# Performance work log

Measured on AMD Instinct MI355X. Metric: run time of the kernel, lower is better.

Reference implementation:

```python
import jax, jax.numpy as jnp
import numpy as np

B, T, D, U = 32, 2048, 512, 512

def setup_inputs() -> dict:
    key = jax.random.key(0)
    ks = jax.random.split(key, 8)
    s = 0.02
    return {
        "query": jax.random.normal(ks[0], (B, D), dtype=jnp.float32),
        "values": jax.random.normal(ks[1], (B, T, D), dtype=jnp.float32),
        "W1_w": jax.random.normal(ks[2], (D, U), dtype=jnp.float32) * s,
        "W1_b": jnp.zeros((U,), dtype=jnp.float32),
        "W2_w": jax.random.normal(ks[3], (D, U), dtype=jnp.float32) * s,
        "W2_b": jnp.zeros((U,), dtype=jnp.float32),
        "V_w": jax.random.normal(ks[4], (U, 1), dtype=jnp.float32) * s,
        "V_b": jnp.zeros((1,), dtype=jnp.float32),
    }

def reference(query, values, W1_w, W1_b, W2_w, W2_b, V_w, V_b):
    # query: [B, D] -> [B, 1, U]; values: [B, T, D] -> [B, T, U]
    q_proj = (query @ W1_w + W1_b)[:, None, :]              # [B, 1, U]
    v_proj = jnp.einsum('btd,du->btu', values, W2_w) + W2_b  # [B, T, U]
    score = jnp.tanh(q_proj + v_proj) @ V_w + V_b            # [B, T, 1]
    attn = jax.nn.softmax(score, axis=1)                     # [B, T, 1]
    context = jnp.sum(attn * values, axis=1)                 # [B, D]
    return context, attn
```

## Files before the change

### kernel.cpp

```cpp
#include <hip/hip_runtime.h>
#include <hip/hip_bf16.h>
#include <cstddef>
#include <cstdint>

#define B_ 32
#define T_ 2048
#define D_ 512
#define U_ 512

typedef __attribute__((ext_vector_type(8))) short bf16x8;
typedef __attribute__((ext_vector_type(4))) float f32x4;

__device__ __forceinline__ unsigned short f2bf(float f) {
  union { float f; unsigned u; } x; x.f = f;
  unsigned r = x.u + 0x7fffu + ((x.u >> 16) & 1u);
  return (unsigned short)(r >> 16);
}
__device__ __forceinline__ float tanh_fast(float x) {
  float e = __expf(2.0f * x);
  return 1.0f - 2.0f * __builtin_amdgcn_rcpf(e + 1.0f);
}

#define AS1C(p) ((const __attribute__((address_space(1))) unsigned*)(p))
#define AS3(p)  ((__attribute__((address_space(3))) unsigned*)(p))

__device__ __forceinline__ void wave0_sumabs_vw(const float* __restrict__ Vw,
                                                float* Cs, int tid) {
  if (tid < 64) {
    float c = 0.f;
    #pragma unroll
    for (int i = 0; i < 8; ++i) c += fabsf(Vw[tid + i * 64]);
    c += __shfl_xor(c, 1);  c += __shfl_xor(c, 2);  c += __shfl_xor(c, 4);
    c += __shfl_xor(c, 8);  c += __shfl_xor(c, 16); c += __shfl_xor(c, 32);
    if (tid == 0) *Cs = c;
  }
}

__global__ void kA_prep(const float* __restrict__ W2, unsigned* __restrict__ W2P,
                        const float* __restrict__ query, const float* __restrict__ W1,
                        const float* __restrict__ W1b, const float* __restrict__ W2b,
                        float* __restrict__ qp, float* __restrict__ ctx) {
  const int tid = threadIdx.x;
  if (blockIdx.x < 64) {
    const int kg = blockIdx.x >> 2, q4 = blockIdx.x & 3;
    __shared__ unsigned short w2s[8][514];
    const float4* W2v = (const float4*)(W2 + (size_t)(kg * 32 + q4 * 8) * U_);
    #pragma unroll
    for (int i = 0; i < 4; ++i) {
      int idx4 = i * 256 + tid;
      float4 v = W2v[idx4];
      int r = idx4 >> 7, c = (idx4 & 127) * 4;
      w2s[r][c + 0] = f2bf(v.x); w2s[r][c + 1] = f2bf(v.y);
      w2s[r][c + 2] = f2bf(v.z); w2s[r][c + 3] = f2bf(v.w);
    }
    __syncthreads();
    const int idx = tid & 63;
    const int lr = (idx >> 2) & 15, j = idx & 3;
    const int kb = j * 2;
    #pragma unroll
    for (int r = 0; r < 8; ++r) {
      int ut = r * 4 + (tid >> 6);
      W2P[ut * 4096 + kg * 256 + q4 * 64 + idx] =
          (unsigned)w2s[kb][ut * 16 + lr] | ((unsigned)w2s[kb + 1][ut * 16 + lr] << 16);
    }
  } else {
    __shared__ float qs[D_];
    __shared__ float red[4][64];
    const int blk2 = blockIdx.x - 64;
    const int b = blk2 >> 3, us = blk2 & 7;
    const int ul = tid & 63, dq = tid >> 6;
    const int u = us * 64 + ul;
    qs[tid] = query[b * D_ + tid];
    qs[tid + 256] = query[b * D_ + tid + 256];
    __syncthreads();
    float a0 = 0, a1 = 0, a2 = 0, a3 = 0;
    const int d0 = dq * 128;
    for (int d = 0; d < 128; d += 4) {
      a0 += qs[d0 + d + 0] * W1[(size_t)(d0 + d + 0) * U_ + u];
      a1 += qs[d0 + d + 1] * W1[(size_t)(d0 + d + 1) * U_ + u];
      a2 += qs[d0 + d + 2] * W1[(size_t)(d0 + d + 2) * U_ + u];
      a3 += qs[d0 + d + 3] * W1[(size_t)(d0 + d + 3) * U_ + u];
    }
    red[dq][ul] = (a0 + a1) + (a2 + a3);
    __syncthreads();
    if (dq == 0) {
      float s = red[0][ul] + red[1][ul] + red[2][ul] + red[3][ul];
      qp[b * U_ + u] = s + W1b[u] + W2b[u];
    }
    if (tid < 64) ctx[blk2 * 64 + tid] = 0.0f;
  }
}

__global__ __launch_bounds__(512, 4) void k2attn(
    const float* __restrict__ values, const unsigned short* __restrict__ W2P,
    const float* __restrict__ qp, const float* __restrict__ Vw,
    float* __restrict__ score, float* __restrict__ ctxU) {
  __shared__ __align__(16) float av[2][4096];
  __shared__ float sred[8][64];
  __shared__ float ps2[64];
  __shared__ float Cs;

  const int tid = threadIdx.x;
  const int bx = blockIdx.x;
  const int m0 = bx * 64;
  const int b = m0 >> 11;
  const int l = tid & 63, w = tid >> 6;
  const int lr = l & 15, lq = l >> 4;

  const int r0 = tid >> 4;
  const int c0 = tid & 15;
  const float* vsrc0 = values + (size_t)(m0 + r0) * D_ + (c0 ^ (r0 & 15)) * 4;
  const float* vsrc1 = values + (size_t)(m0 + 32 + r0) * D_ + (c0 ^ (r0 & 15)) * 4;

  f32x4 acc[4][4];
  #pragma unroll
  for (int mi = 0; mi < 4; ++mi)
    #pragma unroll
    for (int ni = 0; ni < 4; ++ni) acc[mi][ni] = (f32x4){0.f, 0.f, 0.f, 0.f};

  const unsigned short* Bb = W2P + (size_t)(w * 4) * 8192 + (size_t)l * 8;

  auto stage = [&](int e, int p) {
    __builtin_amdgcn_global_load_lds(AS1C(vsrc0 + e * 64), AS3(&av[p][(r0) * 64 + ((tid & 15) << 2)]), 16, 0, 0);
    __builtin_amdgcn_global_load_lds(AS1C(vsrc1 + e * 64), AS3(&av[p][(32 + r0) * 64 + ((tid & 15) << 2)]), 16, 0, 0);
  };

  wave0_sumabs_vw(Vw, &Cs, tid);

  bf16x8 Bc[4], Bn[4];
  stage(0, 0);
  #pragma unroll
  for (int ni = 0; ni < 4; ++ni) Bc[ni] = *(const bf16x8*)(Bb + (size_t)ni * 8192);

  for (int kg = 0; kg < 16; ++kg) {
    const int e = kg >> 1, p = e & 1;
    if ((kg & 1) == 0) {
      __syncthreads();
      if (e < 7) stage(e + 1, p ^ 1);
    }
    if (kg < 15) {
      #pragma unroll
      for (int ni = 0; ni < 4; ++ni)
        Bn[ni] = *(const bf16x8*)(Bb + (size_t)ni * 8192 + (size_t)(kg + 1) * 512);
    }
    const int kq = kg & 1;
    const int p0 = (kq * 8 + lq * 2) ^ lr;
    bf16x8 a[4];
    #pragma unroll
    for (int mi = 0; mi < 4; ++mi) {
      const int row = mi * 16 + lr;
      f32x4 flo = *(const f32x4*)&av[p][row * 64 + (p0 << 2)];
      f32x4 fhi = *(const f32x4*)&av[p][row * 64 + ((p0 ^ 1) << 2)];
      union { bf16x8 v; __hip_bfloat162 h[4]; } A;
      A.h[0] = __float22bfloat162_rn(make_float2(flo.x, flo.y));
      A.h[1] = __float22bfloat162_rn(make_float2(flo.z, flo.w));
      A.h[2] = __float22bfloat162_rn(make_float2(fhi.x, fhi.y));
      A.h[3] = __float22bfloat162_rn(make_float2(fhi.z, fhi.w));
      a[mi] = A.v;
    }
    #pragma unroll
    for (int ni = 0; ni < 4; ++ni)
      #pragma unroll
      for (int mi = 0; mi < 4; ++mi)
        acc[mi][ni] = __builtin_amdgcn_mfma_f32_16x16x32_bf16(a[mi], Bc[ni], acc[mi][ni], 0, 0, 0);
    #pragma unroll
    for (int ni = 0; ni < 4; ++ni) Bc[ni] = Bn[ni];
  }

  float sacc[4][4];
  #pragma unroll
  for (int mi = 0; mi < 4; ++mi)
    #pragma unroll
    for (int r = 0; r < 4; ++r) sacc[mi][r] = 0.0f;
  #pragma unroll
  for (int ni = 0; ni < 4; ++ni) {
    int u = (w * 4 + ni) * 16 + lr;
    float qpv = qp[b * U_ + u], vv = Vw[u];
    #pragma unroll
    for (int mi = 0; mi < 4; ++mi)
      #pragma unroll
      for (int r = 0; r < 4; ++r)
        sacc[mi][r] += tanh_fast(acc[mi][ni][r] + qpv) * vv;
  }
  #pragma unroll
  for (int mi = 0; mi < 4; ++mi)
    #pragma unroll
    for (int r = 0; r < 4; ++r) {
      float v = sacc[mi][r];
      v += __shfl_xor(v, 1); v += __shfl_xor(v, 2);
      v += __shfl_xor(v, 4); v += __shfl_xor(v, 8);
      if (lr == 0) sred[w][mi * 16 + lq * 4 + r] = v;
    }
  __syncthreads();

  if (tid < 64) {
    float s = 0.f;
    #pragma unroll
    for (int wv = 0; wv < 8; ++wv) s += sred[wv][tid];
    score[m0 + tid] = s;
    ps2[tid] = __expf(s - Cs);
  }
  __syncthreads();

  float accc = 0.f;
  const int col = tid;
  #pragma unroll 4
  for (int row = 0; row < 64; ++row)
    accc += ps2[row] * values[(size_t)(m0 + row) * D_ + col];
  atomicAdd(&ctxU[(size_t)b * D_ + col], accc);
}

__global__ void kB_final(const float* __restrict__ Vw, float* __restrict__ attn,
                         float* __restrict__ ctx) {
  __shared__ float Cs;
  __shared__ float red[4];
  const int b = blockIdx.x, tid = threadIdx.x;
  wave0_sumabs_vw(Vw, &Cs, tid);
  __syncthreads();
  const float C = Cs;
  float* s = attn + b * T_;
  float p[8];
  float sum = 0.f;
  #pragma unroll
  for (int i = 0; i < 8; ++i) { p[i] = __expf(s[tid + i * 256] - C); sum += p[i]; }
  #pragma unroll
  for (int off = 1; off < 64; off <<= 1) sum += __shfl_xor(sum, off);
  if ((tid & 63) == 0) red[tid >> 6] = sum;
  __syncthreads();
  sum = (red[0] + red[1]) + (red[2] + red[3]);
  const float inv = 1.0f / sum;
  #pragma unroll
  for (int i = 0; i < 8; ++i) attn[b * T_ + tid + i * 256] = p[i] * inv;
  #pragma unroll
  for (int i = 0; i < 2; ++i) ctx[b * D_ + tid + i * 256] *= inv;
}

extern "C" void kernel_launch(void* const* d_in, const int* in_sizes, int n_in,
                              void* d_out, int out_size, void* d_ws, size_t ws_size,
                              hipStream_t stream) {
  const float* query = (const float*)d_in[0];
  const float* values = (const float*)d_in[1];
  const float* W1w = (const float*)d_in[2];
  const float* W1b = (const float*)d_in[3];
  const float* W2w = (const float*)d_in[4];
  const float* W2b = (const float*)d_in[5];
  const float* Vw  = (const float*)d_in[6];

  float* out = (float*)d_out;
  float* ctx  = out;
  float* attn = out + B_ * D_;
  float* score = attn;

  char* ws = (char*)d_ws;
  unsigned* W2P = (unsigned*)ws;
  float* qp    = (float*)(ws + 512 * 1024);

  kA_prep<<<320, 256, 0, stream>>>(W2w, W2P, query, W1w, W1b, W2b, qp, ctx);
  k2attn<<<1024, 512, 0, stream>>>(values, (const unsigned short*)W2P, qp, Vw, score, ctx);
  kB_final<<<32, 256, 0, stream>>>(Vw, attn, ctx);
}
```

Before: 242.0 us.

## Load A operand directly from global memory instead of LDS staging

Removes the double-buffered LDS staging of the values tile via global_load_lds and its per-stage barriers. Each wave now reads its fp32 A fragments straight from global memory, converts them to bf16, and fully unrolls the k loop with per-iteration B loads. This drops LDS traffic and synchronisation, but every one of the 8 waves now re-reads the same 64-row values tile from global/L2, so redundant global loads go up. The explicit B register prefetch is also removed.

```diff
diff --git a/kernel.cpp b/kernel.cpp
--- a/kernel.cpp
+++ b/kernel.cpp
@@ -20,9 +20,6 @@
   float e = __expf(2.0f * x);
   return 1.0f - 2.0f * __builtin_amdgcn_rcpf(e + 1.0f);
 }
-
-#define AS1C(p) ((const __attribute__((address_space(1))) unsigned*)(p))
-#define AS3(p)  ((__attribute__((address_space(3))) unsigned*)(p))
 
 __device__ __forceinline__ void wave0_sumabs_vw(const float* __restrict__ Vw,
                                                 float* Cs, int tid) {
@@ -91,11 +88,20 @@
   }
 }
 
+#define LOADA(dst, base)                                                  \
+  { f32x4 flo = *(const f32x4*)((base) + kg * 32);                        \
+    f32x4 fhi = *(const f32x4*)((base) + kg * 32 + 4);                    \
+    union { bf16x8 v; __hip_bfloat162 h[4]; } Au;                         \
+    Au.h[0] = __float22bfloat162_rn(make_float2(flo.x, flo.y));           \
+    Au.h[1] = __float22bfloat162_rn(make_float2(flo.z, flo.w));           \
+    Au.h[2] = __float22bfloat162_rn(make_float2(fhi.x, fhi.y));           \
+    Au.h[3] = __float22bfloat162_rn(make_float2(fhi.z, fhi.w));           \
+    dst = Au.v; }
+
 __global__ __launch_bounds__(512, 4) void k2attn(
     const float* __restrict__ values, const unsigned short* __restrict__ W2P,
     const float* __restrict__ qp, const float* __restrict__ Vw,
     float* __restrict__ score, float* __restrict__ ctxU) {
-  __shared__ __align__(16) float av[2][4096];
   __shared__ float sred[8][64];
   __shared__ float ps2[64];
   __shared__ float Cs;
@@ -107,11 +113,6 @@
   const int l = tid & 63, w = tid >> 6;
   const int lr = l & 15, lq = l >> 4;
 
-  const int r0 = tid >> 4;
-  const int c0 = tid & 15;
-  const float* vsrc0 = values + (size_t)(m0 + r0) * D_ + (c0 ^ (r0 & 15)) * 4;
-  const float* vsrc1 = values + (size_t)(m0 + 32 + r0) * D_ + (c0 ^ (r0 & 15)) * 4;
-
   f32x4 acc[4][4];
   #pragma unroll
   for (int mi = 0; mi < 4; ++mi)
@@ -119,52 +120,28 @@
     for (int ni = 0; ni < 4; ++ni) acc[mi][ni] = (f32x4){0.f, 0.f, 0.f, 0.f};
 
   const unsigned short* Bb = W2P + (size_t)(w * 4) * 8192 + (size_t)l * 8;
-
-  auto stage = [&](int e, int p) {
-    __builtin_amdgcn_global_load_lds(AS1C(vsrc0 + e * 64), AS3(&av[p][(r0) * 64 + ((tid & 15) << 2)]), 16, 0, 0);
-    __builtin_amdgcn_global_load_lds(AS1C(vsrc1 + e * 64), AS3(&av[p][(32 + r0) * 64 + ((tid & 15) << 2)]), 16, 0, 0);
-  };
+  const float* a0p = values + (size_t)(m0 + lr) * D_ + lq * 8;
+  const float* a1p = a0p + (size_t)16 * D_;
+  const float* a2p = a0p + (size_t)32 * D_;
+  const float* a3p = a0p + (size_t)48 * D_;
 
   wave0_sumabs_vw(Vw, &Cs, tid);
 
-  bf16x8 Bc[4], Bn[4];
-  stage(0, 0);
-  #pragma unroll
-  for (int ni = 0; ni < 4; ++ni) Bc[ni] = *(const bf16x8*)(Bb + (size_t)ni * 8192);
-
+  #pragma unroll
   for (int kg = 0; kg < 16; ++kg) {
-    const int e = kg >> 1, p = e & 1;
-    if ((kg & 1) == 0) {
-      __syncthreads();
-      if (e < 7) stage(e + 1, p ^ 1);
-    }
-    if (kg < 15) {
-      #pragma unroll
-      for (int ni = 0; ni < 4; ++ni)
-        Bn[ni] = *(const bf16x8*)(Bb + (size_t)ni * 8192 + (size_t)(kg + 1) * 512);
-    }
-    const int kq = kg & 1;
-    const int p0 = (kq * 8 + lq * 2) ^ lr;
-    bf16x8 a[4];
-    #pragma unroll
-    for (int mi = 0; mi < 4; ++mi) {
-      const int row = mi * 16 + lr;
-      f32x4 flo = *(const f32x4*)&av[p][row * 64 + (p0 << 2)];
-      f32x4 fhi = *(const f32x4*)&av[p][row * 64 + ((p0 ^ 1) << 2)];
-      union { bf16x8 v; __hip_bfloat162 h[4]; } A;
-      A.h[0] = __float22bfloat162_rn(make_float2(flo.x, flo.y));
-      A.h[1] = __float22bfloat162_rn(make_float2(flo.z, flo.w));
-      A.h[2] = __float22bfloat162_rn(make_float2(fhi.x, fhi.y));
-      A.h[3] = __float22bfloat162_rn(make_float2(fhi.z, fhi.w));
-      a[mi] = A.v;
-    }
+    bf16x8 Bv[4];
     #pragma unroll
     for (int ni = 0; ni < 4; ++ni)
-      #pragma unroll
-      for (int mi = 0; mi < 4; ++mi)
-        acc[mi][ni] = __builtin_amdgcn_mfma_f32_16x16x32_bf16(a[mi], Bc[ni], acc[mi][ni], 0, 0, 0);
-    #pragma unroll
-    for (int ni = 0; ni < 4; ++ni) Bc[ni] = Bn[ni];
+      Bv[ni] = *(const bf16x8*)(Bb + (size_t)ni * 8192 + (size_t)kg * 512);
+    bf16x8 af0, af1, af2, af3;
+    LOADA(af0, a0p); LOADA(af1, a1p); LOADA(af2, a2p); LOADA(af3, a3p);
+    #pragma unroll
+    for (int ni = 0; ni < 4; ++ni) {
+      acc[0][ni] = __builtin_amdgcn_mfma_f32_16x16x32_bf16(af0, Bv[ni], acc[0][ni], 0, 0, 0);
+      acc[1][ni] = __builtin_amdgcn_mfma_f32_16x16x32_bf16(af1, Bv[ni], acc[1][ni], 0, 0, 0);
+      acc[2][ni] = __builtin_amdgcn_mfma_f32_16x16x32_bf16(af2, Bv[ni], acc[2][ni], 0, 0, 0);
+      acc[3][ni] = __builtin_amdgcn_mfma_f32_16x16x32_bf16(af3, Bv[ni], acc[3][ni], 0, 0, 0);
+    }
   }
 
   float sacc[4][4];
```

New measurement: 357.8 us. 47.9% more time.

## Stage values tile as bf16 in LDS via register prefetch instead of direct fp32 loads

Applied to the files above, without the earlier changes.

Replaces the direct global-to-LDS fp32 staging of the values tile with register-prefetched global loads that are converted to bf16 once and written into a swizzled 64x128 bf16 LDS buffer. Each k-stage now covers 128 columns, processed as four stages of four MFMA k-groups with two register prefetch buffers. This removes the per-wave repeated fp32-to-bf16 conversion and halves LDS footprint and read traffic. In exchange it uses more VGPRs for the prefetch registers, which is why the occupancy hint drops from 4 to 3 blocks per CU, and it gives up the asynchronous load-to-LDS path.

```diff
diff --git a/kernel.cpp b/kernel.cpp
--- a/kernel.cpp
+++ b/kernel.cpp
@@ -20,9 +20,11 @@
   float e = __expf(2.0f * x);
   return 1.0f - 2.0f * __builtin_amdgcn_rcpf(e + 1.0f);
 }
-
-#define AS1C(p) ((const __attribute__((address_space(1))) unsigned*)(p))
-#define AS3(p)  ((__attribute__((address_space(3))) unsigned*)(p))
+__device__ __forceinline__ unsigned packbf2(float a, float b) {
+  union { __hip_bfloat162 h; unsigned u; } c;
+  c.h = __float22bfloat162_rn(make_float2(a, b));
+  return c.u;
+}
 
 __device__ __forceinline__ void wave0_sumabs_vw(const float* __restrict__ Vw,
                                                 float* Cs, int tid) {
@@ -91,11 +93,11 @@
   }
 }
 
-__global__ __launch_bounds__(512, 4) void k2attn(
+__global__ __launch_bounds__(512, 3) void k2attn(
     const float* __restrict__ values, const unsigned short* __restrict__ W2P,
     const float* __restrict__ qp, const float* __restrict__ Vw,
     float* __restrict__ score, float* __restrict__ ctxU) {
-  __shared__ __align__(16) float av[2][4096];
+  __shared__ __align__(16) unsigned short av[2][64][128];
   __shared__ float sred[8][64];
   __shared__ float ps2[64];
   __shared__ float Cs;
@@ -107,10 +109,12 @@
   const int l = tid & 63, w = tid >> 6;
   const int lr = l & 15, lq = l >> 4;
 
-  const int r0 = tid >> 4;
-  const int c0 = tid & 15;
-  const float* vsrc0 = values + (size_t)(m0 + r0) * D_ + (c0 ^ (r0 & 15)) * 4;
-  const float* vsrc1 = values + (size_t)(m0 + 32 + r0) * D_ + (c0 ^ (r0 & 15)) * 4;
+  const int r_st = tid >> 3;
+  const int s0 = (tid & 7) * 2;
+  const int r15 = r_st & 15;
+  const float* gsrc = values + (size_t)(m0 + r_st) * D_ + s0 * 8;
+  char* wd0 = (char*)&av[0][r_st][0] + ((s0 ^ r15) << 4);
+  char* wd1 = (char*)&av[0][r_st][0] + (((s0 + 1) ^ r15) << 4);
 
   f32x4 acc[4][4];
   #pragma unroll
@@ -120,51 +124,64 @@
 
   const unsigned short* Bb = W2P + (size_t)(w * 4) * 8192 + (size_t)l * 8;
 
-  auto stage = [&](int e, int p) {
-    __builtin_amdgcn_global_load_lds(AS1C(vsrc0 + e * 64), AS3(&av[p][(r0) * 64 + ((tid & 15) << 2)]), 16, 0, 0);
-    __builtin_amdgcn_global_load_lds(AS1C(vsrc1 + e * 64), AS3(&av[p][(32 + r0) * 64 + ((tid & 15) << 2)]), 16, 0, 0);
+  float4 La[4], Lb[4];
+  auto loadG = [&](float4* L, int q) {
+    const float4* g = (const float4*)(gsrc + q * 128);
+    L[0] = g[0]; L[1] = g[1]; L[2] = g[2]; L[3] = g[3];
   };
+  auto writeL = [&](int p, const float4* L) {
+    uint4 w0 = make_uint4(packbf2(L[0].x, L[0].y), packbf2(L[0].z, L[0].w),
+                          packbf2(L[1].x, L[1].y), packbf2(L[1].z, L[1].w));
+    uint4 w1 = make_uint4(packbf2(L[2].x, L[2].y), packbf2(L[2].z, L[2].w),
+                          packbf2(L[3].x, L[3].y), packbf2(L[3].z, L[3].w));
+    *(uint4*)(wd0 + p * 16384) = w0;
+    *(uint4*)(wd1 + p * 16384) = w1;
+  };
 
   wave0_sumabs_vw(Vw, &Cs, tid);
 
+  loadG(La, 0);
+  writeL(0, La);
+  loadG(Lb, 1);
+  __syncthreads();
+
   bf16x8 Bc[4], Bn[4];
-  stage(0, 0);
   #pragma unroll
   for (int ni = 0; ni < 4; ++ni) Bc[ni] = *(const bf16x8*)(Bb + (size_t)ni * 8192);
 
-  for (int kg = 0; kg < 16; ++kg) {
-    const int e = kg >> 1, p = e & 1;
-    if ((kg & 1) == 0) {
+  #pragma unroll
+  for (int q = 0; q < 4; ++q) {
+    const int p = q & 1;
+    if (q == 0) loadG(La, 2);
+    else if (q == 1) loadG(Lb, 3);
+    const char* buf = (const char*)av[p];
+    #pragma unroll
+    for (int kgl = 0; kgl < 4; ++kgl) {
+      const int kg = q * 4 + kgl;
+      if (kg < 15) {
+        #pragma unroll
+        for (int ni = 0; ni < 4; ++ni)
+          Bn[ni] = *(const bf16x8*)(Bb + (size_t)ni * 8192 + (size_t)(kg + 1) * 512);
+      }
+      bf16x8 a[4];
+      #pragma unroll
+      for (int mi = 0; mi < 4; ++mi) {
+        const int row = mi * 16 + lr;
+        const int phys = (kgl * 4 + lq) ^ lr;
+        a[mi] = *(const bf16x8*)(buf + row * 256 + (phys << 4));
+      }
+      #pragma unroll
+      for (int ni = 0; ni < 4; ++ni)
+        #pragma unroll
+        for (int mi = 0; mi < 4; ++mi)
+          acc[mi][ni] = __builtin_amdgcn_mfma_f32_16x16x32_bf16(a[mi], Bc[ni], acc[mi][ni], 0, 0, 0);
+      #pragma unroll
+      for (int ni = 0; ni < 4; ++ni) Bc[ni] = Bn[ni];
+    }
+    if (q < 3) {
+      writeL(p ^ 1, (q & 1) ? La : Lb);
       __syncthreads();
-      if (e < 7) stage(e + 1, p ^ 1);
-    }
-    if (kg < 15) {
-      #pragma unroll
-      for (int ni = 0; ni < 4; ++ni)
-        Bn[ni] = *(const bf16x8*)(Bb + (size_t)ni * 8192 + (size_t)(kg + 1) * 512);
-    }
-    const int kq = kg & 1;
-    const int p0 = (kq * 8 + lq * 2) ^ lr;
-    bf16x8 a[4];
-    #pragma unroll
-    for (int mi = 0; mi < 4; ++mi) {
-      const int row = mi * 16 + lr;
-      f32x4 flo = *(const f32x4*)&av[p][row * 64 + (p0 << 2)];
-      f32x4 fhi = *(const f32x4*)&av[p][row * 64 + ((p0 ^ 1) << 2)];
-      union { bf16x8 v; __hip_bfloat162 h[4]; } A;
-      A.h[0] = __float22bfloat162_rn(make_float2(flo.x, flo.y));
-      A.h[1] = __float22bfloat162_rn(make_float2(flo.z, flo.w));
-      A.h[2] = __float22bfloat162_rn(make_float2(fhi.x, fhi.y));
-      A.h[3] = __float22bfloat162_rn(make_float2(fhi.z, fhi.w));
-      a[mi] = A.v;
-    }
-    #pragma unroll
-    for (int ni = 0; ni < 4; ++ni)
-      #pragma unroll
-      for (int mi = 0; mi < 4; ++mi)
-        acc[mi][ni] = __builtin_amdgcn_mfma_f32_16x16x32_bf16(a[mi], Bc[ni], acc[mi][ni], 0, 0, 0);
-    #pragma unroll
-    for (int ni = 0; ni < 4; ++ni) Bc[ni] = Bn[ni];
+    }
   }
 
   float sacc[4][4];
```

Measured after the change: 266.9 us. 1.1x slower.
